# Kernel tuning notes

Measured on AMD Instinct MI355X. Metric: run time of the kernel, lower is better.

## Reference

```python
import jax, jax.numpy as jnp
import numpy as np
import math

BS, N, D_MODEL, H = 8, 1024, 512, 8
D_K = D_MODEL // H


def setup_inputs() -> dict:
    key = jax.random.key(0)
    ks = jax.random.split(key, 12)
    s = 1.0 / math.sqrt(D_MODEL)
    inp = {
        "query": jax.random.normal(ks[0], (BS, N, D_MODEL), jnp.float32),
        "key": jax.random.normal(ks[1], (BS, N, D_MODEL), jnp.float32),
        "value": jax.random.normal(ks[2], (BS, N, D_MODEL), jnp.float32),
        "wc_matrix": jax.random.normal(ks[3], (BS, N, N), jnp.float32),
        "Wq": jax.random.normal(ks[4], (D_MODEL, D_MODEL), jnp.float32) * s,
        "bq": jnp.zeros((D_MODEL,), jnp.float32),
        "Wk": jax.random.normal(ks[5], (D_MODEL, D_MODEL), jnp.float32) * s,
        "bk": jnp.zeros((D_MODEL,), jnp.float32),
        "Wv": jax.random.normal(ks[6], (D_MODEL, D_MODEL), jnp.float32) * s,
        "bv": jnp.zeros((D_MODEL,), jnp.float32),
        "Wo": jax.random.normal(ks[7], (D_MODEL, D_MODEL), jnp.float32) * s,
        "bo": jnp.zeros((D_MODEL,), jnp.float32),
    }
    return inp


def _split_heads(x):
    # (bs, N, d_model) -> (bs, h, N, d_k)
    b, n, _ = x.shape
    return x.reshape(b, n, H, D_K).transpose(0, 2, 1, 3)


def reference(query, key, value, wc_matrix, Wq, bq, Wk, bk, Wv, bv, Wo, bo):
    # Linear projections (torch Linear: x @ W.T + b), split into heads
    q = _split_heads(query @ Wq.T + bq)
    k = _split_heads(key @ Wk.T + bk)
    v = _split_heads(value @ Wv.T + bv)

    # scores: (bs, h, N, N)
    scores = jnp.einsum("bhnd,bhmd->bhnm", q, k) / jnp.sqrt(jnp.float32(D_K))
    # WC modulation: scores * softmax(wc)[:, None] + scores  (softmax_wc=True, residual=True)
    wc_sm = jax.nn.softmax(wc_matrix, axis=-1)[:, None]  # (bs, 1, N, N)
    scores = scores * wc_sm + scores
    p_attn = jax.nn.softmax(scores, axis=-1)  # dropout is identity in eval

    a = jnp.einsum("bhnm,bhmd->bhnd", p_attn, v)
    a = a.transpose(0, 2, 1, 3).reshape(query.shape[0], -1, D_MODEL)
    return a @ Wo.T + bo
```

## Files before the change

kernel.cpp:

```cpp
#include <hip/hip_runtime.h>
#include <math.h>


#define BS 8
#define SEQ 1024
#define DM 512
#define NH 8
#define DK 64
#define ROWS (BS * SEQ)

typedef __bf16 bf16_t;
typedef bf16_t bf16x8 __attribute__((ext_vector_type(8)));
typedef bf16_t bf16x4 __attribute__((ext_vector_type(4)));
typedef float f32x4 __attribute__((ext_vector_type(4)));

__device__ inline f32x4 mfma32(bf16x8 a, bf16x8 b, f32x4 c) {
  return __builtin_amdgcn_mfma_f32_16x16x32_bf16(a, b, c, 0, 0, 0);
}

__device__ inline void gload_lds16(const bf16_t* g, bf16_t* l) {
  __builtin_amdgcn_global_load_lds(
      (const __attribute__((address_space(1))) void*)g,
      (__attribute__((address_space(3))) void*)l, 16, 0, 0);
}

__global__ __launch_bounds__(256) void cvt_kernel(
    const float* q, const float* k, const float* v,
    const float* wq, const float* wk, const float* wv, const float* wo,
    bf16_t* xq, bf16_t* xk, bf16_t* xv,
    bf16_t* wqb, bf16_t* wkb, bf16_t* wvb, bf16_t* wob) {
  const float* srcs[7] = {q, k, v, wq, wk, wv, wo};
  bf16_t* dsts[7] = {xq, xk, xv, wqb, wkb, wvb, wob};
  int b = blockIdx.x;
  int seg, boff;
  if (b < 1536) { seg = b >> 9; boff = b & 511; }
  else { seg = 3 + ((b - 1536) >> 5); boff = (b - 1536) & 31; }
  const float* src = srcs[seg] + (size_t)boff * 8192;
  bf16_t* dst = dsts[seg] + (size_t)boff * 8192;
  int t = threadIdx.x;
#pragma unroll
  for (int f = 0; f < 8; ++f) {
    int idx = (f * 256 + t) * 4;
    float4 x = *(const float4*)(src + idx);
    bf16x4 o;
    o[0] = (bf16_t)x.x; o[1] = (bf16_t)x.y; o[2] = (bf16_t)x.z; o[3] = (bf16_t)x.w;
    *(bf16x4*)(dst + idx) = o;
  }
}

__global__ __launch_bounds__(256) void wc_softmax_kernel(const float* __restrict__ wc,
                                                         bf16_t* __restrict__ G) {
  int row = blockIdx.x;
  const float* x = wc + (size_t)row * SEQ;
  bf16_t* y = G + (size_t)row * SEQ;
  int t = threadIdx.x;
  float4 v = *(const float4*)(x + t * 4);
  float m = fmaxf(fmaxf(v.x, v.y), fmaxf(v.z, v.w));
#pragma unroll
  for (int off = 32; off > 0; off >>= 1) m = fmaxf(m, __shfl_xor(m, off, 64));
  __shared__ float sm[4], ss[4];
  int w = t >> 6;
  if ((t & 63) == 0) sm[w] = m;
  __syncthreads();
  m = fmaxf(fmaxf(sm[0], sm[1]), fmaxf(sm[2], sm[3]));
  float4 e;
  e.x = __expf(v.x - m); e.y = __expf(v.y - m);
  e.z = __expf(v.z - m); e.w = __expf(v.w - m);
  float s = e.x + e.y + e.z + e.w;
#pragma unroll
  for (int off = 32; off > 0; off >>= 1) s += __shfl_xor(s, off, 64);
  if ((t & 63) == 0) ss[w] = s;
  __syncthreads();
  s = ss[0] + ss[1] + ss[2] + ss[3];
  float inv = 1.0f / s;
  bf16x4 g;
  g[0] = (bf16_t)(1.0f + e.x * inv);
  g[1] = (bf16_t)(1.0f + e.y * inv);
  g[2] = (bf16_t)(1.0f + e.z * inv);
  g[3] = (bf16_t)(1.0f + e.w * inv);
  *(bf16x4*)(y + t * 4) = g;
}

template <int BM, bool OUTF32>
__device__ inline void gemm_core(const bf16_t* X, const bf16_t* W,
                                 const float* bias, void* Cv,
                                 int mblk, int nblk) {
  __shared__ bf16_t As[BM * 32];
  __shared__ bf16_t Bs[128 * 32];
  int t = threadIdx.x, lane = t & 63, w = t >> 6;
  int quad = lane >> 4, l15 = lane & 15;
  constexpr int MT = BM / 32;
  int m0w = (w & 1) * (BM / 2), n0w = (w >> 1) * 64;
  int mbase = mblk * BM, nbase = nblk * 128;
  int lr = lane >> 2, l4 = lane & 3;
  f32x4 acc[MT][4] = {};

  for (int kb = 0; kb < DM; kb += 32) {
    __syncthreads();
#pragma unroll
    for (int f = 0; f < BM / 64; ++f) {
      int i = f * 4 + w;
      gload_lds16(X + (size_t)(mbase + i * 16 + lr) * DM + kb + l4 * 8, As + i * 512);
    }
#pragma unroll
    for (int f = 0; f < 2; ++f) {
      int i = f * 4 + w;
      gload_lds16(W + (size_t)(nbase + i * 16 + lr) * DM + kb + l4 * 8, Bs + i * 512);
    }
    __syncthreads();
    bf16x8 af[MT], bf[4];
#pragma unroll
    for (int mt = 0; mt < MT; ++mt)
      af[mt] = *(const bf16x8*)&As[(m0w + mt * 16 + l15) * 32 + quad * 8];
#pragma unroll
    for (int nt = 0; nt < 4; ++nt)
      bf[nt] = *(const bf16x8*)&Bs[(n0w + nt * 16 + l15) * 32 + quad * 8];
#pragma unroll
    for (int mt = 0; mt < MT; ++mt)
#pragma unroll
      for (int nt = 0; nt < 4; ++nt)
        acc[mt][nt] = mfma32(af[mt], bf[nt], acc[mt][nt]);
  }

#pragma unroll
  for (int nt = 0; nt < 4; ++nt) {
    int col = nbase + n0w + nt * 16 + l15;
    float bc = bias[col];
#pragma unroll
    for (int mt = 0; mt < MT; ++mt)
#pragma unroll
      for (int r = 0; r < 4; ++r) {
        int row = mbase + m0w + mt * 16 + quad * 4 + r;
        float vv = acc[mt][nt][r] + bc;
        if (OUTF32)
          ((float*)Cv)[(size_t)row * DM + col] = vv;
        else
          ((bf16_t*)Cv)[(size_t)row * DM + col] = (bf16_t)vv;
      }
  }
}

__global__ __launch_bounds__(256) void gemm_qkv_kernel(
    const bf16_t* xq, const bf16_t* xk, const bf16_t* xv,
    const bf16_t* wq, const bf16_t* wk, const bf16_t* wv,
    const float* bq, const float* bk, const float* bv,
    bf16_t* cq, bf16_t* ck, bf16_t* cv) {
  const bf16_t* Xarr[3] = {xq, xk, xv};
  const bf16_t* Warr[3] = {wq, wk, wv};
  const float* barr[3] = {bq, bk, bv};
  bf16_t* Carr[3] = {cq, ck, cv};
  int z = blockIdx.z;
  gemm_core<128, false>(Xarr[z], Warr[z], barr[z], Carr[z], blockIdx.x, blockIdx.y);
}

__global__ __launch_bounds__(256) void gemm_wo_kernel(const bf16_t* X, const bf16_t* W,
                                                      const float* bias, float* C) {
  gemm_core<64, true>(X, W, bias, C, blockIdx.x, blockIdx.y);
}

__global__ __launch_bounds__(256) void vtrans_kernel(const bf16_t* __restrict__ Vb,
                                                     bf16_t* __restrict__ Vt) {
  int mt = blockIdx.x;
  int bh = blockIdx.y;
  int b = bh >> 3, h = bh & 7;
  __shared__ bf16_t Ts[64][66];
  int t = threadIdx.x;
#pragma unroll
  for (int f = 0; f < 2; ++f) {
    int chunk = t + f * 256;
    int row = chunk >> 3;
    int c8 = (chunk & 7) * 8;
    bf16x8 v = *(const bf16x8*)&Vb[(size_t)(b * SEQ + mt * 64 + row) * DM + h * DK + c8];
#pragma unroll
    for (int j = 0; j < 8; ++j) Ts[c8 + j][row] = v[j];
  }
  __syncthreads();
#pragma unroll
  for (int f = 0; f < 2; ++f) {
    int chunk = t + f * 256;
    int d = chunk >> 3;
    int m8 = (chunk & 7) * 8;
    bf16x8 o;
#pragma unroll
    for (int j = 0; j < 8; ++j) o[j] = Ts[d][m8 + j];
    *(bf16x8*)&Vt[((size_t)(bh * DK + d)) * SEQ + mt * 64 + m8] = o;
  }
}

__global__ __launch_bounds__(256) void flash_mfma_kernel(const bf16_t* __restrict__ Qb,
                                                         const bf16_t* __restrict__ Kb,
                                                         const bf16_t* __restrict__ Vt,
                                                         const bf16_t* __restrict__ G,
                                                         bf16_t* __restrict__ Ab) {
  int qt = blockIdx.x, h = blockIdx.y, b = blockIdx.z;
  __shared__ bf16_t Qs[64][72];
  __shared__ bf16_t Ks[64][72];
  __shared__ bf16_t Vs[64][72];
  __shared__ bf16_t Ps[64][72];
  int t = threadIdx.x, lane = t & 63, w = t >> 6;
  int quad = lane >> 4, l15 = lane & 15;

#pragma unroll
  for (int f = 0; f < 2; ++f) {
    int chunk = t + f * 256;
    int row = chunk >> 3, k8 = (chunk & 7) * 8;
    *(bf16x8*)&Qs[row][k8] =
        *(const bf16x8*)&Qb[(size_t)(b * SEQ + qt * 64 + row) * DM + h * DK + k8];
  }
  __syncthreads();
  bf16x8 aq0 = *(const bf16x8*)&Qs[w * 16 + l15][quad * 8];
  bf16x8 aq1 = *(const bf16x8*)&Qs[w * 16 + l15][32 + quad * 8];

  float m_st = -INFINITY, l_st = 0.f;
  f32x4 o[4] = {};
  const size_t grow = (size_t)(b * SEQ + qt * 64 + w * 16 + l15) * SEQ;

  for (int mt = 0; mt < 16; ++mt) {
    __syncthreads();
#pragma unroll
    for (int f = 0; f < 2; ++f) {
      int chunk = t + f * 256;
      int row = chunk >> 3, k8 = (chunk & 7) * 8;
      *(bf16x8*)&Ks[row][k8] =
          *(const bf16x8*)&Kb[(size_t)(b * SEQ + mt * 64 + row) * DM + h * DK + k8];
      *(bf16x8*)&Vs[row][k8] =
          *(const bf16x8*)&Vt[((size_t)((b * NH + h) * DK + row)) * SEQ + mt * 64 + k8];
    }
    __syncthreads();

    f32x4 s[4];
#pragma unroll
    for (int ct = 0; ct < 4; ++ct) {
      bf16x8 ak0 = *(const bf16x8*)&Ks[ct * 16 + l15][quad * 8];
      bf16x8 ak1 = *(const bf16x8*)&Ks[ct * 16 + l15][32 + quad * 8];
      f32x4 z = {};
      s[ct] = mfma32(ak1, aq1, mfma32(ak0, aq0, z));
    }

    float sv[4][4];
    float rm = -INFINITY;
#pragma unroll
    for (int ct = 0; ct < 4; ++ct) {
      bf16x4 g4 = *(const bf16x4*)&G[grow + mt * 64 + ct * 16 + quad * 4];
#pragma unroll
      for (int r = 0; r < 4; ++r) {
        float x = s[ct][r] * 0.125f * (float)g4[r];
        sv[ct][r] = x;
        rm = fmaxf(rm, x);
      }
    }
    rm = fmaxf(rm, __shfl_xor(rm, 16, 64));
    rm = fmaxf(rm, __shfl_xor(rm, 32, 64));
    float mnew = fmaxf(m_st, rm);
    float alpha = __expf(m_st - mnew);
    m_st = mnew;

    float rs = 0.f;
#pragma unroll
    for (int ct = 0; ct < 4; ++ct) {
      bf16x4 pb;
#pragma unroll
      for (int r = 0; r < 4; ++r) {
        float p = __expf(sv[ct][r] - mnew);
        pb[r] = (bf16_t)p;
        rs += p;
      }
      *(bf16x4*)&Ps[w * 16 + l15][ct * 16 + quad * 4] = pb;
    }
    rs += __shfl_xor(rs, 16, 64);
    rs += __shfl_xor(rs, 32, 64);
    l_st = l_st * alpha + rs;

#pragma unroll
    for (int dt = 0; dt < 4; ++dt) {
      o[dt][0] *= alpha; o[dt][1] *= alpha; o[dt][2] *= alpha; o[dt][3] *= alpha;
    }
#pragma unroll
    for (int c = 0; c < 2; ++c) {
      bf16x8 bp = *(const bf16x8*)&Ps[w * 16 + l15][c * 32 + quad * 8];
#pragma unroll
      for (int dt = 0; dt < 4; ++dt) {
        bf16x8 av = *(const bf16x8*)&Vs[dt * 16 + l15][c * 32 + quad * 8];
        o[dt] = mfma32(av, bp, o[dt]);
      }
    }
  }

  float linv = 1.0f / l_st;
  size_t qrow = (size_t)(b * SEQ + qt * 64 + w * 16 + l15);
#pragma unroll
  for (int dt = 0; dt < 4; ++dt)
#pragma unroll
    for (int r = 0; r < 4; ++r)
      Ab[qrow * DM + h * DK + dt * 16 + quad * 4 + r] = (bf16_t)(o[dt][r] * linv);
}

extern "C" void kernel_launch(void* const* d_in, const int* in_sizes, int n_in,
                              void* d_out, int out_size, void* d_ws, size_t ws_size,
                              hipStream_t stream) {
  const float* query = (const float*)d_in[0];
  const float* key = (const float*)d_in[1];
  const float* value = (const float*)d_in[2];
  const float* wc = (const float*)d_in[3];
  const float* Wq = (const float*)d_in[4];
  const float* bq = (const float*)d_in[5];
  const float* Wk = (const float*)d_in[6];
  const float* bk = (const float*)d_in[7];
  const float* Wv = (const float*)d_in[8];
  const float* bv = (const float*)d_in[9];
  const float* Wo = (const float*)d_in[10];
  const float* bo = (const float*)d_in[11];
  float* out = (float*)d_out;

  const size_t ACT = (size_t)ROWS * DM;
  const size_t WSZ = (size_t)DM * DM;
  bf16_t* Qb = (bf16_t*)d_ws;
  bf16_t* Kb = Qb + ACT;
  bf16_t* Vb = Kb + ACT;
  bf16_t* Vt = Vb + ACT;
  bf16_t* Ab = Vt + ACT;
  bf16_t* G = Ab + ACT;
  bf16_t* Xq = G + (size_t)BS * SEQ * SEQ;
  bf16_t* Xk = Xq + ACT;
  bf16_t* Xv = Xk + ACT;
  bf16_t* Wqb = Xv + ACT;
  bf16_t* Wkb = Wqb + WSZ;
  bf16_t* Wvb = Wkb + WSZ;
  bf16_t* Wob = Wvb + WSZ;

  cvt_kernel<<<1664, 256, 0, stream>>>(query, key, value, Wq, Wk, Wv, Wo,
                                       Xq, Xk, Xv, Wqb, Wkb, Wvb, Wob);

  wc_softmax_kernel<<<BS * SEQ, 256, 0, stream>>>(wc, G);

  gemm_qkv_kernel<<<dim3(ROWS / 128, DM / 128, 3), 256, 0, stream>>>(
      Xq, Xk, Xv, Wqb, Wkb, Wvb, bq, bk, bv, Qb, Kb, Vb);

  vtrans_kernel<<<dim3(16, 64), 256, 0, stream>>>(Vb, Vt);

  flash_mfma_kernel<<<dim3(SEQ / 64, NH, BS), 256, 0, stream>>>(Qb, Kb, Vt, G, Ab);

  gemm_wo_kernel<<<dim3(ROWS / 64, DM / 128), 256, 0, stream>>>(Ab, Wob, bo, out);
}
```

Baseline: 241.3 us.

## Double-buffer GEMM LDS tiles and register-prefetch K/V/gate tiles in attention

The projection GEMM now uses two LDS buffers and issues the next k-slice's global_load_lds before computing on the current one, which drops one barrier per iteration. The attention kernel prefetches the next K, V and gate tiles into registers while the current tile is computed, so global load latency overlaps with MFMA and softmax work. The cost is doubled LDS in the GEMM and extra registers in attention, which may lower occupancy. The GEMM loop relies on the asynchronous LDS load being complete by the next barrier without an explicit vmcnt wait, which could be a correctness risk.

```diff
diff --git a/kernel.cpp b/kernel.cpp
--- a/kernel.cpp
+++ b/kernel.cpp
@@ -85,8 +85,8 @@
 __device__ inline void gemm_core(const bf16_t* X, const bf16_t* W,
                                  const float* bias, void* Cv,
                                  int mblk, int nblk) {
-  __shared__ bf16_t As[BM * 32];
-  __shared__ bf16_t Bs[128 * 32];
+  __shared__ bf16_t As[2][BM * 32];
+  __shared__ bf16_t Bs[2][128 * 32];
   int t = threadIdx.x, lane = t & 63, w = t >> 6;
   int quad = lane >> 4, l15 = lane & 15;
   constexpr int MT = BM / 32;
@@ -95,31 +95,45 @@
   int lr = lane >> 2, l4 = lane & 3;
   f32x4 acc[MT][4] = {};
 
-  for (int kb = 0; kb < DM; kb += 32) {
+#pragma unroll
+  for (int f = 0; f < BM / 64; ++f) {
+    int i = f * 4 + w;
+    gload_lds16(X + (size_t)(mbase + i * 16 + lr) * DM + l4 * 8, &As[0][i * 512]);
+  }
+#pragma unroll
+  for (int f = 0; f < 2; ++f) {
+    int i = f * 4 + w;
+    gload_lds16(W + (size_t)(nbase + i * 16 + lr) * DM + l4 * 8, &Bs[0][i * 512]);
+  }
+
+  for (int it = 0; it < 16; ++it) {
     __syncthreads();
-#pragma unroll
-    for (int f = 0; f < BM / 64; ++f) {
-      int i = f * 4 + w;
-      gload_lds16(X + (size_t)(mbase + i * 16 + lr) * DM + kb + l4 * 8, As + i * 512);
-    }
-#pragma unroll
-    for (int f = 0; f < 2; ++f) {
-      int i = f * 4 + w;
-      gload_lds16(W + (size_t)(nbase + i * 16 + lr) * DM + kb + l4 * 8, Bs + i * 512);
-    }
-    __syncthreads();
-    bf16x8 af[MT], bf[4];
+    int cb = it & 1;
+    if (it + 1 < 16) {
+      int kb = (it + 1) * 32, nb = (it + 1) & 1;
+#pragma unroll
+      for (int f = 0; f < BM / 64; ++f) {
+        int i = f * 4 + w;
+        gload_lds16(X + (size_t)(mbase + i * 16 + lr) * DM + kb + l4 * 8, &As[nb][i * 512]);
+      }
+#pragma unroll
+      for (int f = 0; f < 2; ++f) {
+        int i = f * 4 + w;
+        gload_lds16(W + (size_t)(nbase + i * 16 + lr) * DM + kb + l4 * 8, &Bs[nb][i * 512]);
+      }
+    }
+    bf16x8 af[MT], bfr[4];
 #pragma unroll
     for (int mt = 0; mt < MT; ++mt)
-      af[mt] = *(const bf16x8*)&As[(m0w + mt * 16 + l15) * 32 + quad * 8];
+      af[mt] = *(const bf16x8*)&As[cb][(m0w + mt * 16 + l15) * 32 + quad * 8];
 #pragma unroll
     for (int nt = 0; nt < 4; ++nt)
-      bf[nt] = *(const bf16x8*)&Bs[(n0w + nt * 16 + l15) * 32 + quad * 8];
+      bfr[nt] = *(const bf16x8*)&Bs[cb][(n0w + nt * 16 + l15) * 32 + quad * 8];
 #pragma unroll
     for (int mt = 0; mt < MT; ++mt)
 #pragma unroll
       for (int nt = 0; nt < 4; ++nt)
-        acc[mt][nt] = mfma32(af[mt], bf[nt], acc[mt][nt]);
+        acc[mt][nt] = mfma32(af[mt], bfr[nt], acc[mt][nt]);
   }
 
 #pragma unroll
@@ -215,18 +229,41 @@
   f32x4 o[4] = {};
   const size_t grow = (size_t)(b * SEQ + qt * 64 + w * 16 + l15) * SEQ;
 
+  int srow[2], sk8[2];
+#pragma unroll
+  for (int f = 0; f < 2; ++f) {
+    int chunk = t + f * 256;
+    srow[f] = chunk >> 3;
+    sk8[f] = (chunk & 7) * 8;
+  }
+  const bf16_t* Kbase = Kb + (size_t)b * SEQ * DM + h * DK;
+  const bf16_t* Vbase = Vt + (size_t)(b * NH + h) * DK * SEQ;
+  bf16x8 kreg[2], vreg[2];
+  bf16x4 greg[4];
+#pragma unroll
+  for (int f = 0; f < 2; ++f) {
+    kreg[f] = *(const bf16x8*)&Kbase[(size_t)srow[f] * DM + sk8[f]];
+    vreg[f] = *(const bf16x8*)&Vbase[(size_t)srow[f] * SEQ + sk8[f]];
+  }
+#pragma unroll
+  for (int ct = 0; ct < 4; ++ct)
+    greg[ct] = *(const bf16x4*)&G[grow + ct * 16 + quad * 4];
+
   for (int mt = 0; mt < 16; ++mt) {
     __syncthreads();
 #pragma unroll
     for (int f = 0; f < 2; ++f) {
-      int chunk = t + f * 256;
-      int row = chunk >> 3, k8 = (chunk & 7) * 8;
-      *(bf16x8*)&Ks[row][k8] =
-          *(const bf16x8*)&Kb[(size_t)(b * SEQ + mt * 64 + row) * DM + h * DK + k8];
-      *(bf16x8*)&Vs[row][k8] =
-          *(const bf16x8*)&Vt[((size_t)((b * NH + h) * DK + row)) * SEQ + mt * 64 + k8];
+      *(bf16x8*)&Ks[srow[f]][sk8[f]] = kreg[f];
+      *(bf16x8*)&Vs[srow[f]][sk8[f]] = vreg[f];
     }
     __syncthreads();
+    if (mt + 1 < 16) {
+#pragma unroll
+      for (int f = 0; f < 2; ++f) {
+        kreg[f] = *(const bf16x8*)&Kbase[(size_t)((mt + 1) * 64 + srow[f]) * DM + sk8[f]];
+        vreg[f] = *(const bf16x8*)&Vbase[(size_t)srow[f] * SEQ + (mt + 1) * 64 + sk8[f]];
+      }
+    }
 
     f32x4 s[4];
 #pragma unroll
@@ -241,13 +278,17 @@
     float rm = -INFINITY;
 #pragma unroll
     for (int ct = 0; ct < 4; ++ct) {
-      bf16x4 g4 = *(const bf16x4*)&G[grow + mt * 64 + ct * 16 + quad * 4];
 #pragma unroll
       for (int r = 0; r < 4; ++r) {
-        float x = s[ct][r] * 0.125f * (float)g4[r];
+        float x = s[ct][r] * 0.125f * (float)greg[ct][r];
         sv[ct][r] = x;
         rm = fmaxf(rm, x);
       }
+    }
+    if (mt + 1 < 16) {
+#pragma unroll
+      for (int ct = 0; ct < 4; ++ct)
+        greg[ct] = *(const bf16x4*)&G[grow + (mt + 1) * 64 + ct * 16 + quad * 4];
     }
     rm = fmaxf(rm, __shfl_xor(rm, 16, 64));
     rm = fmaxf(rm, __shfl_xor(rm, 32, 64));
```

New measurement: 230.0 us. 4.7% less time.
